# Performance work log

Measured on AMD Instinct MI355X. Metric: run time of the kernel, lower is better.

Reference implementation:

```python
import jax, jax.numpy as jnp
import numpy as np
from jax.scipy.special import logsumexp

S, L = 32768, 512  # seq_len, label_num


def setup_inputs() -> dict:
    key = jax.random.key(0)
    k1, k2, k3 = jax.random.split(key, 3)
    logit = jax.random.normal(k1, (S, L), dtype=jnp.float32)   # emissions [S, L]
    labels = jax.random.randint(k2, (S,), 0, L)                # gold path [S]
    T = jax.random.normal(k3, (L, L), dtype=jnp.float32)       # T[next, prev]
    return {"logit": logit, "labels": labels, "T": T}


def _crf_loss(logit, T, labels):
    # Forward algorithm: alpha_t[j] = logsumexp_i(alpha_{t-1}[i] + T[j, i]) + feat_t[j]
    alpha0 = logit[0]

    def step(alpha, feat):
        new_alpha = logsumexp(alpha[None, :] + T, axis=1) + feat  # [L]
        return new_alpha, None

    alpha_final, _ = jax.lax.scan(step, alpha0, logit[1:])
    log_Z = logsumexp(alpha_final)

    # Gold path score: feat_0[y0] + sum_{t>0} (feat_t[y_t] + T[y_t, y_{t-1}])
    emit = logit[0, labels[0]] + jnp.sum(logit[jnp.arange(1, logit.shape[0]), labels[1:]])
    trans = jnp.sum(T[labels[1:], labels[:-1]])
    gold = emit + trans
    return log_Z - gold


def reference(logit, labels, T):
    return _crf_loss(logit, T, labels)
```

## Files before the change

kernel.cpp:

```cpp
#include <hip/hip_runtime.h>
#include <stdint.h>


#define S_LEN 32768
#define L 512
#define CH 16
#define NCF 2048
#define WGF 128
#define WGB 128
#define NWG 256
#define LN448 6.104793232f
#define LN2   0.6931471806f

#define OFF_EAF  0
#define OFF_EAB  (256*1024)
#define OFF_G    (512*1024)
#define OFF_H    (OFF_G + NCF*L*2)
#define OFF_LSE  (OFF_H + NCF*L*2)
#define OFF_PART (OFF_LSE + 4100*4)
#define OFF_PTKT (OFF_PART + 256*4)
#define OFF_FTKT (OFF_PTKT + 128*4)

#define BAR_LDS() asm volatile("s_waitcnt lgkmcnt(0)\n\ts_barrier" ::: "memory")

typedef float v4f __attribute__((ext_vector_type(4)));

__device__ __forceinline__ float b2f(unsigned short u){
  return __uint_as_float(((unsigned)u) << 16);
}
__device__ __forceinline__ unsigned short f2b(float x){
  unsigned u = __float_as_uint(x);
  return (unsigned short)((u + 0x7fffu + ((u >> 16) & 1u)) >> 16);
}
__device__ __forceinline__ unsigned char to_fp8(float v){
  int u = __builtin_amdgcn_cvt_pk_fp8_f32(v, v, 0, false);
  return (unsigned char)(u & 0xff);
}

extern "C" __global__ void crf_prep(const float* __restrict__ T,
                                    unsigned char* __restrict__ EAf,
                                    unsigned char* __restrict__ EAb,
                                    unsigned int* __restrict__ ptkt,
                                    unsigned int* __restrict__ ftkt){
  int tid = blockIdx.x*512 + threadIdx.x;
  if (tid < 129) { if (tid < 128) ptkt[tid] = 0u; else *ftkt = 0u; }
  int r    = tid & 7;
  int lane = (tid >> 3) & 63;
  int kt   = (tid >> 9) & 15;
  int mtw  = tid >> 13;
  int j = (mtw >> 2)*64 + (mtw & 3)*16 + (lane & 15);
  int i = kt*32 + ((lane >> 4) << 3) + r;
  EAf[tid] = to_fp8(2.0f * __expf(T[j*L + i]));
  EAb[tid] = to_fp8(2.0f * __expf(T[i*L + j]));
}

__device__ __forceinline__ float blockSum(float v, float* sred){
  #pragma unroll
  for (int off = 32; off >= 1; off >>= 1) v += __shfl_xor(v, off);
  int wid = threadIdx.x >> 6, lane = threadIdx.x & 63;
  if (lane == 0) sred[wid] = v;
  __syncthreads();
  if (threadIdx.x < 8) {
    float t = sred[threadIdx.x];
    t += __shfl_xor(t, 4); t += __shfl_xor(t, 2); t += __shfl_xor(t, 1);
    if (threadIdx.x == 0) sred[15] = t;
  }
  __syncthreads();
  float r = sred[15];
  __syncthreads();
  return r;
}

extern "C" __global__ __launch_bounds__(512, 2)
void crf_chunks(const float* __restrict__ logit,
                const unsigned char* __restrict__ EAf,
                const unsigned char* __restrict__ EAb,
                unsigned short* __restrict__ G, unsigned short* __restrict__ H,
                const int* __restrict__ labels, const float* __restrict__ T,
                float* __restrict__ part, float* __restrict__ lsebuf,
                unsigned int* __restrict__ ptkt, unsigned int* __restrict__ ftkt,
                float* __restrict__ out){
  __shared__ __align__(16) unsigned char Pl[2][8192];
  __shared__ float sPart[16][8];
  __shared__ float sred[16];
  __shared__ unsigned sOld, sOld2;

  const int tid  = threadIdx.x;
  const int w    = tid >> 6;
  const int lane = tid & 63;
  const int quad = lane >> 4;
  const int cl   = lane & 15;
  const bool fwd = (blockIdx.x < WGF);
  const int  b   = fwd ? blockIdx.x : (blockIdx.x - WGF);
  const int  cg  = fwd ? (b*16 + cl) : (1 + b*16 + cl);
  const int  cgc = min(cg, NCF-1);
  const bool isc0 = fwd && (cg == 0);
  const int  jrow0 = w*64 + quad*4;

  const long* EA = (const long*)(fwd ? EAf : EAb);
  long eA[4][16];
  #pragma unroll
  for (int mt = 0; mt < 4; ++mt)
    #pragma unroll
    for (int kt = 0; kt < 16; ++kt)
      eA[mt][kt] = EA[(((w<<2)+mt)<<4 | kt)*64 + lane];

  auto t_of = [&](int k)->int {
    if (fwd) return cgc*CH + min(k, CH-1);
    int kk = CH - 2 - k; if (kk < 0) kk = 0;
    return cgc*CH + kk;
  };

  float4 pfA[4], pfB[4];
  { const float* lp = logit + (size_t)t_of(0)*L + jrow0;
    #pragma unroll
    for (int mt = 0; mt < 4; ++mt) pfA[mt] = *(const float4*)(lp + mt*16); }
  { const float* lp = logit + (size_t)t_of(1)*L + jrow0;
    #pragma unroll
    for (int mt = 0; mt < 4; ++mt) pfB[mt] = *(const float4*)(lp + mt*16); }

  float vr[4][4];
  if (fwd) {
    #pragma unroll
    for (int mt = 0; mt < 4; ++mt)
      #pragma unroll
      for (int r = 0; r < 4; ++r) vr[mt][r] = 1.0f;
  } else {
    const float* lp = logit + (size_t)(cgc*CH + CH - 1)*L + jrow0;
    #pragma unroll
    for (int mt = 0; mt < 4; ++mt) {
      float4 x = *(const float4*)(lp + mt*16);
      vr[mt][0] = __expf(x.x); vr[mt][1] = __expf(x.y);
      vr[mt][2] = __expf(x.z); vr[mt][3] = __expf(x.w);
    }
  }
  float m = 0.0f;

  auto renorm_store = [&](int dst){
    float mx = vr[0][0];
    #pragma unroll
    for (int mt = 0; mt < 4; ++mt)
      #pragma unroll
      for (int r = 0; r < 4; ++r) mx = fmaxf(mx, vr[mt][r]);
    mx = fmaxf(mx, __shfl_xor(mx, 16));
    mx = fmaxf(mx, __shfl_xor(mx, 32));
    if (quad == 0) sPart[cl][w] = mx;
    BAR_LDS();
    float4 pa = *(const float4*)&sPart[cl][0];
    float4 pb = *(const float4*)&sPart[cl][4];
    float M = fmaxf(fmaxf(fmaxf(pa.x,pa.y),fmaxf(pa.z,pa.w)),
                    fmaxf(fmaxf(pb.x,pb.y),fmaxf(pb.z,pb.w)));
    float sc = 448.0f / M;
    #pragma unroll
    for (int mt = 0; mt < 4; ++mt) {
      int u = __builtin_amdgcn_cvt_pk_fp8_f32(vr[mt][0]*sc, vr[mt][1]*sc, 0, false);
      u     = __builtin_amdgcn_cvt_pk_fp8_f32(vr[mt][2]*sc, vr[mt][3]*sc, u, true);
      int r0 = jrow0 + mt*16;
      *(int*)&Pl[dst][(r0 >> 5)*512 + ((((r0 >> 3) & 3)*16 + cl) << 3) + (r0 & 7)] = u;
    }
    m += __logf(M) - LN448;
    BAR_LDS();
  };

  auto step = [&](int k, int rdBuf, int wrBuf, float4 (&pfc)[4]){
    const bool last = (k == CH-1);
    const bool useF = fwd || !last;
    float fex[4][4];
    #pragma unroll
    for (int mt = 0; mt < 4; ++mt) {
      float4 x = pfc[mt];
      fex[mt][0] = __expf(x.x); fex[mt][1] = __expf(x.y);
      fex[mt][2] = __expf(x.z); fex[mt][3] = __expf(x.w);
    }
    { const float* lp = logit + (size_t)t_of(k+2)*L + jrow0;
      #pragma unroll
      for (int mt = 0; mt < 4; ++mt) pfc[mt] = *(const float4*)(lp + mt*16); }

    v4f acc[4];
    #pragma unroll
    for (int mt = 0; mt < 4; ++mt) acc[mt] = (v4f){0.f,0.f,0.f,0.f};
    #pragma unroll
    for (int kt = 0; kt < 16; ++kt) {
      long bb = *(const long*)&Pl[rdBuf][kt*512 + lane*8];
      #pragma unroll
      for (int mt = 0; mt < 4; ++mt)
        acc[mt] = __builtin_amdgcn_mfma_f32_16x16x32_fp8_fp8(eA[mt][kt], bb, acc[mt], 0, 0, 0);
    }
    m -= LN2;

    if (useF) {
      #pragma unroll
      for (int mt = 0; mt < 4; ++mt) {
        vr[mt][0] = acc[mt][0]*fex[mt][0]; vr[mt][1] = acc[mt][1]*fex[mt][1];
        vr[mt][2] = acc[mt][2]*fex[mt][2]; vr[mt][3] = acc[mt][3]*fex[mt][3];
        if (k == 0 && isc0) {
          vr[mt][0] = fex[mt][0]; vr[mt][1] = fex[mt][1];
          vr[mt][2] = fex[mt][2]; vr[mt][3] = fex[mt][3];
        }
      }
      if (k == 0 && isc0) m = 0.0f;
    } else {
      #pragma unroll
      for (int mt = 0; mt < 4; ++mt)
        #pragma unroll
        for (int r = 0; r < 4; ++r) vr[mt][r] = acc[mt][r];
    }

    if (last) {
      if (cg <= NCF-1) {
        unsigned short* dst = (fwd ? G : H) + (size_t)cg*L + jrow0;
        #pragma unroll
        for (int mt = 0; mt < 4; ++mt) {
          ushort4 o;
          o.x = f2b(__logf(vr[mt][0]) + m); o.y = f2b(__logf(vr[mt][1]) + m);
          o.z = f2b(__logf(vr[mt][2]) + m); o.w = f2b(__logf(vr[mt][3]) + m);
          *(ushort4*)(dst + mt*16) = o;
        }
      }
    } else {
      renorm_store(wrBuf);
    }
  };

  renorm_store(0);
  for (int kk = 0; kk < CH; kk += 2) {
    step(kk,     0, 1, pfA);
    step(kk + 1, 1, 0, pfB);
  }

  {
    float gv = 0.f;
    if (tid < 128) {
      int t = blockIdx.x*128 + tid;
      int yt = labels[t];
      gv = logit[(size_t)t*L + yt];
      if (t > 0) gv += T[yt*L + labels[t-1]];
    }
    float s = blockSum(gv, sred);
    if (tid == 0) part[blockIdx.x] = s;
  }

  __syncthreads();
  if (tid == 0) { __threadfence(); sOld = atomicAdd(&ptkt[b], 1u); }
  __syncthreads();
  if (sOld == 1u) {
    __threadfence();
    const int wv = w;
    #pragma unroll
    for (int q = 0; q < 2; ++q) {
      int idx = wv*2 + q;
      int c = b*16 + 1 + idx;
      if (c <= NCF-1) {
        const ushort4* hp = (const ushort4*)(H + (size_t)c*L + lane*8);
        const ushort4* gp = (const ushort4*)(G + (size_t)(c-1)*L + lane*8);
        ushort4 h0 = hp[0], h1 = hp[1], g0 = gp[0], g1 = gp[1];
        float hh[8] = {b2f(h0.x),b2f(h0.y),b2f(h0.z),b2f(h0.w),
                       b2f(h1.x),b2f(h1.y),b2f(h1.z),b2f(h1.w)};
        float aa[8] = {hh[0]+b2f(g0.x),hh[1]+b2f(g0.y),hh[2]+b2f(g0.z),hh[3]+b2f(g0.w),
                       hh[4]+b2f(g1.x),hh[5]+b2f(g1.y),hh[6]+b2f(g1.z),hh[7]+b2f(g1.w)};
        float Ma = aa[0], Mh = hh[0];
        #pragma unroll
        for (int r = 1; r < 8; ++r) { Ma = fmaxf(Ma, aa[r]); Mh = fmaxf(Mh, hh[r]); }
        #pragma unroll
        for (int off = 1; off <= 32; off <<= 1) {
          Ma = fmaxf(Ma, __shfl_xor(Ma, off));
          Mh = fmaxf(Mh, __shfl_xor(Mh, off));
        }
        float sa = 0.f, sh = 0.f;
        #pragma unroll
        for (int r = 0; r < 8; ++r) { sa += __expf(aa[r]-Ma); sh += __expf(hh[r]-Mh); }
        #pragma unroll
        for (int off = 1; off <= 32; off <<= 1) {
          sa += __shfl_xor(sa, off);
          sh += __shfl_xor(sh, off);
        }
        if (lane == 0) { lsebuf[c] = Ma + __logf(sa); lsebuf[NCF + c] = Mh + __logf(sh); }
      } else {
        const ushort4* gp = (const ushort4*)(G + (size_t)(NCF-1)*L + lane*8);
        ushort4 u0 = gp[0], u1 = gp[1];
        float v[8] = {b2f(u0.x),b2f(u0.y),b2f(u0.z),b2f(u0.w),
                      b2f(u1.x),b2f(u1.y),b2f(u1.z),b2f(u1.w)};
        float M = v[0];
        #pragma unroll
        for (int r = 1; r < 8; ++r) M = fmaxf(M, v[r]);
        #pragma unroll
        for (int off = 1; off <= 32; off <<= 1) M = fmaxf(M, __shfl_xor(M, off));
        float s = 0.f;
        #pragma unroll
        for (int r = 0; r < 8; ++r) s += __expf(v[r] - M);
        #pragma unroll
        for (int off = 1; off <= 32; off <<= 1) s += __shfl_xor(s, off);
        if (lane == 0) lsebuf[2*NCF] = M + __logf(s);
      }
    }
  }

  __syncthreads();
  if (tid == 0) { __threadfence(); sOld2 = atomicAdd(ftkt, 1u); }
  __syncthreads();
  if (sOld2 == (unsigned)(NWG - 1)) {
    __threadfence();
    float acc = 0.f;
    for (int c = tid; c < NCF; c += 512)
      if (c >= 1) acc += lsebuf[c] - lsebuf[NCF + c];
    if (tid < NWG) acc -= part[tid];
    float s = blockSum(acc, sred);
    if (tid == 0) out[0] = lsebuf[2*NCF] + s;
  }
}

extern "C" void kernel_launch(void* const* d_in, const int* in_sizes, int n_in,
                              void* d_out, int out_size, void* d_ws, size_t ws_size,
                              hipStream_t stream){
  const float* logit = (const float*)d_in[0];
  const int* labels  = (const int*)d_in[1];
  const float* T     = (const float*)d_in[2];
  float* out = (float*)d_out;
  char* ws = (char*)d_ws;
  unsigned char* EAf = (unsigned char*)(ws + OFF_EAF);
  unsigned char* EAb = (unsigned char*)(ws + OFF_EAB);
  unsigned short* G  = (unsigned short*)(ws + OFF_G);
  unsigned short* H  = (unsigned short*)(ws + OFF_H);
  float* lsebuf = (float*)(ws + OFF_LSE);
  float* part   = (float*)(ws + OFF_PART);
  unsigned int* ptkt = (unsigned int*)(ws + OFF_PTKT);
  unsigned int* ftkt = (unsigned int*)(ws + OFF_FTKT);

  crf_prep  <<<512, 512, 0, stream>>>(T, EAf, EAb, ptkt, ftkt);
  crf_chunks<<<NWG, 512, 0, stream>>>(logit, EAf, EAb, G, H, labels, T,
                                      part, lsebuf, ptkt, ftkt, out);
}
```

Before: 155.6 us.

## Halve CRF chunk length to double workgroups and drop logit prefetch

Cuts the chunk length from 16 to 8 steps. This doubles the number of forward and backward chunks and workgroups (512 total), shortening the serial matrix-chain per workgroup and raising the occupancy hint to 4. The double-buffered register prefetch of logit rows is removed; each step now loads and exponentiates its row inline. The custom LDS-wait barrier is replaced with __syncthreads. The risks are register spills from the large fp8 transition fragments under the higher occupancy bound, exposed global-load latency per step, and twice as many G/H rows and merge work.

```diff
diff --git a/kernel.cpp b/kernel.cpp
--- a/kernel.cpp
+++ b/kernel.cpp
@@ -4,11 +4,11 @@
 
 #define S_LEN 32768
 #define L 512
-#define CH 16
-#define NCF 2048
-#define WGF 128
-#define WGB 128
-#define NWG 256
+#define CH 8
+#define NCF 4096
+#define WGF 256
+#define WGB 256
+#define NWG 512
 #define LN448 6.104793232f
 #define LN2   0.6931471806f
 
@@ -17,11 +17,9 @@
 #define OFF_G    (512*1024)
 #define OFF_H    (OFF_G + NCF*L*2)
 #define OFF_LSE  (OFF_H + NCF*L*2)
-#define OFF_PART (OFF_LSE + 4100*4)
-#define OFF_PTKT (OFF_PART + 256*4)
-#define OFF_FTKT (OFF_PTKT + 128*4)
-
-#define BAR_LDS() asm volatile("s_waitcnt lgkmcnt(0)\n\ts_barrier" ::: "memory")
+#define OFF_PART (OFF_LSE + (2*NCF+4)*4)
+#define OFF_PTKT (OFF_PART + NWG*4)
+#define OFF_FTKT (OFF_PTKT + WGF*4)
 
 typedef float v4f __attribute__((ext_vector_type(4)));
 
@@ -43,7 +41,7 @@
                                     unsigned int* __restrict__ ptkt,
                                     unsigned int* __restrict__ ftkt){
   int tid = blockIdx.x*512 + threadIdx.x;
-  if (tid < 129) { if (tid < 128) ptkt[tid] = 0u; else *ftkt = 0u; }
+  if (tid < WGF + 1) { if (tid < WGF) ptkt[tid] = 0u; else *ftkt = 0u; }
   int r    = tid & 7;
   int lane = (tid >> 3) & 63;
   int kt   = (tid >> 9) & 15;
@@ -71,7 +69,7 @@
   return r;
 }
 
-extern "C" __global__ __launch_bounds__(512, 2)
+extern "C" __global__ __launch_bounds__(512, 4)
 void crf_chunks(const float* __restrict__ logit,
                 const unsigned char* __restrict__ EAf,
                 const unsigned char* __restrict__ EAb,
@@ -105,20 +103,6 @@
     for (int kt = 0; kt < 16; ++kt)
       eA[mt][kt] = EA[(((w<<2)+mt)<<4 | kt)*64 + lane];
 
-  auto t_of = [&](int k)->int {
-    if (fwd) return cgc*CH + min(k, CH-1);
-    int kk = CH - 2 - k; if (kk < 0) kk = 0;
-    return cgc*CH + kk;
-  };
-
-  float4 pfA[4], pfB[4];
-  { const float* lp = logit + (size_t)t_of(0)*L + jrow0;
-    #pragma unroll
-    for (int mt = 0; mt < 4; ++mt) pfA[mt] = *(const float4*)(lp + mt*16); }
-  { const float* lp = logit + (size_t)t_of(1)*L + jrow0;
-    #pragma unroll
-    for (int mt = 0; mt < 4; ++mt) pfB[mt] = *(const float4*)(lp + mt*16); }
-
   float vr[4][4];
   if (fwd) {
     #pragma unroll
@@ -145,7 +129,7 @@
     mx = fmaxf(mx, __shfl_xor(mx, 16));
     mx = fmaxf(mx, __shfl_xor(mx, 32));
     if (quad == 0) sPart[cl][w] = mx;
-    BAR_LDS();
+    __syncthreads();
     float4 pa = *(const float4*)&sPart[cl][0];
     float4 pb = *(const float4*)&sPart[cl][4];
     float M = fmaxf(fmaxf(fmaxf(pa.x,pa.y),fmaxf(pa.z,pa.w)),
@@ -159,22 +143,20 @@
       *(int*)&Pl[dst][(r0 >> 5)*512 + ((((r0 >> 3) & 3)*16 + cl) << 3) + (r0 & 7)] = u;
     }
     m += __logf(M) - LN448;
-    BAR_LDS();
+    __syncthreads();
   };
 
-  auto step = [&](int k, int rdBuf, int wrBuf, float4 (&pfc)[4]){
+  auto step = [&](int k, int rdBuf, int wrBuf){
     const bool last = (k == CH-1);
     const bool useF = fwd || !last;
-    float fex[4][4];
-    #pragma unroll
-    for (int mt = 0; mt < 4; ++mt) {
-      float4 x = pfc[mt];
-      fex[mt][0] = __expf(x.x); fex[mt][1] = __expf(x.y);
-      fex[mt][2] = __expf(x.z); fex[mt][3] = __expf(x.w);
-    }
-    { const float* lp = logit + (size_t)t_of(k+2)*L + jrow0;
-      #pragma unroll
-      for (int mt = 0; mt < 4; ++mt) pfc[mt] = *(const float4*)(lp + mt*16); }
+
+    float4 x0, x1, x2, x3;
+    if (useF) {
+      const int t = fwd ? (cgc*CH + k) : (cgc*CH + CH - 2 - k);
+      const float* lp = logit + (size_t)t*L + jrow0;
+      x0 = *(const float4*)(lp);      x1 = *(const float4*)(lp + 16);
+      x2 = *(const float4*)(lp + 32); x3 = *(const float4*)(lp + 48);
+    }
 
     v4f acc[4];
     #pragma unroll
@@ -189,13 +171,15 @@
     m -= LN2;
 
     if (useF) {
+      float4 xs[4] = {x0, x1, x2, x3};
       #pragma unroll
       for (int mt = 0; mt < 4; ++mt) {
-        vr[mt][0] = acc[mt][0]*fex[mt][0]; vr[mt][1] = acc[mt][1]*fex[mt][1];
-        vr[mt][2] = acc[mt][2]*fex[mt][2]; vr[mt][3] = acc[mt][3]*fex[mt][3];
+        float f0 = __expf(xs[mt].x), f1 = __expf(xs[mt].y);
+        float f2 = __expf(xs[mt].z), f3 = __expf(xs[mt].w);
+        vr[mt][0] = acc[mt][0]*f0; vr[mt][1] = acc[mt][1]*f1;
+        vr[mt][2] = acc[mt][2]*f2; vr[mt][3] = acc[mt][3]*f3;
         if (k == 0 && isc0) {
-          vr[mt][0] = fex[mt][0]; vr[mt][1] = fex[mt][1];
-          vr[mt][2] = fex[mt][2]; vr[mt][3] = fex[mt][3];
+          vr[mt][0] = f0; vr[mt][1] = f1; vr[mt][2] = f2; vr[mt][3] = f3;
         }
       }
       if (k == 0 && isc0) m = 0.0f;
@@ -223,15 +207,16 @@
   };
 
   renorm_store(0);
+  #pragma unroll
   for (int kk = 0; kk < CH; kk += 2) {
-    step(kk,     0, 1, pfA);
-    step(kk + 1, 1, 0, pfB);
+    step(kk,     0, 1);
+    step(kk + 1, 1, 0);
   }
 
   {
     float gv = 0.f;
-    if (tid < 128) {
-      int t = blockIdx.x*128 + tid;
+    if (tid < 64) {
+      int t = blockIdx.x*64 + tid;
       int yt = labels[t];
       gv = logit[(size_t)t*L + yt];
       if (t > 0) gv += T[yt*L + labels[t-1]];
@@ -245,10 +230,9 @@
   __syncthreads();
   if (sOld == 1u) {
     __threadfence();
-    const int wv = w;
     #pragma unroll
     for (int q = 0; q < 2; ++q) {
-      int idx = wv*2 + q;
+      int idx = w*2 + q;
       int c = b*16 + 1 + idx;
       if (c <= NCF-1) {
         const ushort4* hp = (const ushort4*)(H + (size_t)c*L + lane*8);
@@ -303,7 +287,7 @@
     float acc = 0.f;
     for (int c = tid; c < NCF; c += 512)
       if (c >= 1) acc += lsebuf[c] - lsebuf[NCF + c];
-    if (tid < NWG) acc -= part[tid];
+    acc -= part[tid];
     float s = blockSum(acc, sred);
     if (tid == 0) out[0] = lsebuf[2*NCF] + s;
   }
```

Result: slower. 305.3 us (+96.2%).
